# Kernel tuning notes

Measured on AMD Instinct MI355X. Metric: run time of the kernel, lower is better.

The kernel has to match this reference:

```python
import jax, jax.numpy as jnp
from jax import lax
import numpy as np

D_MODEL = 1024
EXPAND = 2
D_INNER = D_MODEL * EXPAND
D_STATE = 16
D_CONV = 4
DECAY = 0.95
LN_EPS = 1e-5


def setup_inputs() -> dict:
    key = jax.random.key(0)
    ks = jax.random.split(key, 9)
    b, s = 4, 2048
    scale = 1.0 / np.sqrt(D_MODEL)
    inner_scale = 1.0 / np.sqrt(D_INNER)
    return {
        "x": jax.random.normal(ks[0], (b, s, D_MODEL), dtype=jnp.float32),
        "W_in": jax.random.normal(ks[1], (2 * D_INNER, D_MODEL), dtype=jnp.float32) * scale,
        "conv_w": jax.random.normal(ks[2], (D_INNER, 1, D_CONV), dtype=jnp.float32) * 0.5,
        "conv_b": jax.random.normal(ks[3], (D_INNER,), dtype=jnp.float32) * 0.1,
        "W_x": jax.random.normal(ks[4], (2 * D_STATE, D_INNER), dtype=jnp.float32) * inner_scale,
        "B_log": jax.random.normal(ks[5], (D_INNER, D_STATE), dtype=jnp.float32) * 0.05,  # xavier-ish small
        "W_out": jax.random.normal(ks[6], (D_MODEL, D_INNER), dtype=jnp.float32) * inner_scale,
        "ln_g": jnp.ones((D_MODEL,), dtype=jnp.float32),
        "ln_b": jnp.zeros((D_MODEL,), dtype=jnp.float32),
    }


def _ssm_block(x, W_in, conv_w, conv_b, W_x, B_log, W_out, ln_g, ln_b):
    b, s, _ = x.shape
    d_inner = W_in.shape[0] // 2
    d_conv = conv_w.shape[-1]

    # input projection and gate split
    xz = jnp.einsum('bsd,ed->bse', x, W_in)            # [b, s, 2*d_inner]
    x_inner, z = jnp.split(xz, 2, axis=-1)             # each [b, s, d_inner]

    # causal depthwise conv (left pad d_conv-1, output length s)
    xc = jnp.transpose(x_inner, (0, 2, 1))             # [b, d_inner, s]
    conv = lax.conv_general_dilated(
        xc, conv_w, window_strides=(1,), padding=[(d_conv - 1, 0)],
        feature_group_count=d_inner)
    conv = conv + conv_b[None, :, None]
    x_conv = jax.nn.silu(jnp.transpose(conv, (0, 2, 1)))  # [b, s, d_inner]

    # selective parameters; s_B is produced but unused in the original math
    sp = jnp.einsum('bsd,nd->bsn', x_conv, W_x)        # [b, s, 2*d_state]
    _s_B, s_C = jnp.split(sp, 2, axis=-1)              # each [b, s, d_state]

    B = jnp.exp(B_log)                                  # [d_inner, d_state]

    # state_t = 0.95*state_{t-1} + B * x_t  factorizes as  state = B[d,n]*h[b,t,d]
    # with h_t = 0.95*h_{t-1} + x_conv_t ; scan over time with [b, d_inner] carry.
    def step(h, xt):
        h = DECAY * h + xt
        return h, h

    h0 = jnp.zeros((b, d_inner), dtype=x.dtype)
    _, h = lax.scan(step, h0, jnp.swapaxes(x_conv, 0, 1))  # [s, b, d_inner]
    h = jnp.swapaxes(h, 0, 1)                              # [b, s, d_inner]

    # output_t[b,d] = sum_n state[b,d,n]*s_C[b,t,n] = h[b,t,d] * (s_C @ B^T)[b,t,d]
    y = h * jnp.einsum('bsn,dn->bsd', s_C, B)
    y = y * jax.nn.silu(z)
    y = jnp.einsum('bsd,od->bso', y, W_out)            # [b, s, d_model]

    resid = x + y
    mu = jnp.mean(resid, axis=-1, keepdims=True)
    var = jnp.var(resid, axis=-1, keepdims=True)
    return (resid - mu) * lax.rsqrt(var + LN_EPS) * ln_g + ln_b


def reference(x, W_in, conv_w, conv_b, W_x, B_log, W_out, ln_g, ln_b):
    return _ssm_block(x, W_in, conv_w, conv_b, W_x, B_log, W_out, ln_g, ln_b)
```

## Files before the change

kernel.cpp:

```cpp
#include <hip/hip_runtime.h>
#include <hip/hip_bf16.h>
#include <stdint.h>

#define DM   1024
#define DI   2048
#define NST  16
#define BSZ  4
#define SLEN 2048
#define MROWS (BSZ*SLEN)
#define CHUNK 32
#define NCH  (SLEN/CHUNK)
#define DECAYF 0.95f
#define MB (size_t)1048576

typedef _Float16 f16;
typedef __attribute__((ext_vector_type(2))) _Float16 f16x2;
typedef __attribute__((ext_vector_type(4))) _Float16 f16x4;
typedef __attribute__((ext_vector_type(8))) _Float16 f16x8;
typedef __attribute__((ext_vector_type(4))) float f32x4;

__device__ __forceinline__ float silu_f(float v) { return v / (1.f + __expf(-v)); }

__device__ __forceinline__ void gload16(const f16* lds, const f16* g) {
  __builtin_amdgcn_global_load_lds((const __attribute__((address_space(1))) void*)g,
                                   (__attribute__((address_space(3))) void*)lds, 16, 0, 0);
}

#define NX4  (MROWS * DM / 4)
#define NWI4 (2 * DI * DM / 4)
#define NWO4 (DM * DI / 4)
#define NWX4 (NST * DI / 4)
#define NE4  (NST * DI / 4)
__global__ __launch_bounds__(256) void cvt_all(
    const float* __restrict__ x, const float* __restrict__ wi, const float* __restrict__ wo,
    const float* __restrict__ Wx, const float* __restrict__ B_log,
    f16* __restrict__ A1, f16* __restrict__ B1, f16* __restrict__ W2,
    f16* __restrict__ WxC, f16* __restrict__ expBT)
{
  int i = blockIdx.x * 256 + threadIdx.x;
  if (i < NX4 + NWI4 + NWO4 + NWX4) {
    const float* src; f16* dst; int j;
    if (i < NX4)                     { src = x;  dst = A1; j = i; }
    else if (i < NX4 + NWI4)         { src = wi; dst = B1; j = i - NX4; }
    else if (i < NX4 + NWI4 + NWO4)  { src = wo; dst = W2; j = i - NX4 - NWI4; }
    else                             { src = Wx + (size_t)NST * DI; dst = WxC; j = i - NX4 - NWI4 - NWO4; }
    float4 v = ((const float4*)src)[j];
    f16x4 o = {(f16)v.x, (f16)v.y, (f16)v.z, (f16)v.w};
    ((f16x4*)dst)[j] = o;
  } else {
    int j = i - NX4 - NWI4 - NWO4 - NWX4;
    int base = j * 4;
    int n = base >> 11, d = base & (DI - 1);
    f16x4 o = {(f16)__expf(B_log[(d + 0) * NST + n]), (f16)__expf(B_log[(d + 1) * NST + n]),
               (f16)__expf(B_log[(d + 2) * NST + n]), (f16)__expf(B_log[(d + 3) * NST + n])};
    ((f16x4*)expBT)[j] = o;
  }
}

#define G1K 1024

__device__ __forceinline__ void stage_t(const f16* __restrict__ mat, int matBase,
                                        int kt, f16* ldsDst, int tid) {
  #pragma unroll
  for (int q = 0; q < 2; ++q) {
    int c = q * 512 + tid;
    int row = c >> 2, p = c & 3;
    int su = p ^ ((row >> 1) & 3);
    gload16(ldsDst + c * 8, mat + (size_t)(matBase + row) * G1K + kt * 32 + su * 8);
  }
}

#define WAITV(n) asm volatile("s_waitcnt vmcnt(" #n ")" ::: "memory")

__global__ __launch_bounds__(512, 2) void gemm1_8ph(
    const f16* __restrict__ A, const f16* __restrict__ Bt,
    f16* __restrict__ Xi, f16* __restrict__ Zs)
{
  __shared__ __align__(16) f16 lds[65536];
  const int tid  = threadIdx.x;
  const int lane = tid & 63;
  const int w    = tid >> 6;
  const int wr   = w >> 2, wc = w & 3;
  const int lr   = lane & 15;
  const int lq   = lane >> 4;

  const int nwg = gridDim.x * gridDim.y;
  int wgid = blockIdx.y * gridDim.x + blockIdx.x;
  wgid = (wgid & 7) * (nwg >> 3) + (wgid >> 3);
  const int bx = wgid % gridDim.x;
  const int by = wgid / gridDim.x;
  const int mBase = by * 256;
  const int nBase = bx * 256;

  f32x4 acc[8][4];
  #pragma unroll
  for (int mf = 0; mf < 8; ++mf)
    #pragma unroll
    for (int nf = 0; nf < 4; ++nf)
      acc[mf][nf] = (f32x4){0.f, 0.f, 0.f, 0.f};

  auto rdA = [&](int S, int mf) -> f16x8 {
    int ra = wr * 128 + mf * 16 + lr;
    return *(const f16x8*)&lds[S + ra * 32 + (lq ^ ((ra >> 1) & 3)) * 8];
  };
  auto rdB = [&](int S, int nf) -> f16x8 {
    int rb = wc * 64 + nf * 16 + lr;
    return *(const f16x8*)&lds[S + 8192 + rb * 32 + (lq ^ ((rb >> 1) & 3)) * 8];
  };

  f16x8 bfr[4], afr[8];

#define PH(S, ISSUE, TAIL) do {                                                 \
    _Pragma("unroll")                                                           \
    for (int nf = 0; nf < 4; ++nf) bfr[nf] = rdB((S), nf);                      \
    _Pragma("unroll")                                                           \
    for (int mm = 0; mm < 8; ++mm) afr[mm] = rdA((S), mm);                      \
    ISSUE;                                                                      \
    __builtin_amdgcn_s_barrier();                                               \
    asm volatile("s_waitcnt lgkmcnt(0)" ::: "memory");                          \
    __builtin_amdgcn_sched_barrier(0);                                          \
    __builtin_amdgcn_s_setprio(1);                                              \
    _Pragma("unroll")                                                           \
    for (int mm = 0; mm < 8; ++mm)                                              \
      _Pragma("unroll")                                                         \
      for (int nf = 0; nf < 4; ++nf)                                            \
        acc[mm][nf] = __builtin_amdgcn_mfma_f32_16x16x32_f16(                   \
            afr[mm], bfr[nf], acc[mm][nf], 0, 0, 0);                            \
    __builtin_amdgcn_s_setprio(0);                                              \
    __builtin_amdgcn_sched_barrier(0);                                          \
    TAIL;                                                                       \
    __builtin_amdgcn_s_barrier();                                               \
  } while (0)

  stage_t(A,  mBase, 0, &lds[0],             tid);
  stage_t(Bt, nBase, 0, &lds[8192],          tid);
  stage_t(A,  mBase, 1, &lds[16384],         tid);
  stage_t(Bt, nBase, 1, &lds[16384 + 8192],  tid);
  stage_t(A,  mBase, 2, &lds[32768],         tid);
  stage_t(Bt, nBase, 2, &lds[32768 + 8192],  tid);
  WAITV(8);
  __builtin_amdgcn_s_barrier();

  #pragma unroll
  for (int T = 0; T < 32; ++T) {
    const int S = (T & 3) * 16384;
    const int F = ((T + 3) & 3) * 16384;
    PH(S,
       { if (T + 3 < 32) { stage_t(A, mBase, T + 3, &lds[F], tid);
                           stage_t(Bt, nBase, T + 3, &lds[F + 8192], tid); } },
       { if (T < 29) { WAITV(8); } else if (T == 29) { WAITV(4); } else if (T == 30) { WAITV(0); } });
  }
#undef PH

  __syncthreads();
  const int rq = lq * 4;
  #pragma unroll
  for (int mf = 0; mf < 8; ++mf)
    #pragma unroll
    for (int nf = 0; nf < 4; ++nf)
      #pragma unroll
      for (int r = 0; r < 4; ++r)
        lds[(wr * 128 + mf * 16 + rq + r) * 256 + wc * 64 + nf * 16 + lr] = (f16)acc[mf][nf][r];
  __syncthreads();
  #pragma unroll
  for (int it = 0; it < 16; ++it) {
    int cidx = it * 512 + tid;
    int row = cidx >> 5;
    int col8 = (cidx & 31) * 8;
    int grow = mBase + row;
    int gcol = nBase + col8;
    f16x8 v = *(const f16x8*)&lds[row * 256 + col8];
    if (gcol < DI) *(f16x8*)&Xi[(size_t)grow * DI + gcol] = v;
    else           *(f16x8*)&Zs[(size_t)grow * DI + (gcol - DI)] = v;
  }
}

template<int MODE>
__global__ __launch_bounds__(256) void gemm_bt(
    const f16* __restrict__ A, const f16* __restrict__ Bt,
    int K, f16* __restrict__ O0, f16* __restrict__ O1)
{
  __shared__ __align__(16) f16 sA[128 * 64];
  __shared__ __align__(16) f16 sB[128 * 64];
  const int tid  = threadIdx.x;
  const int lane = tid & 63;
  const int w    = tid >> 6;
  const int wr   = w >> 1, wc = w & 1;

  const int nwg  = gridDim.x * gridDim.y;
  int wgid = blockIdx.y * gridDim.x + blockIdx.x;
  wgid = (wgid & 7) * (nwg >> 3) + (wgid >> 3);
  const int bx = wgid % gridDim.x;
  const int by = wgid / gridDim.x;

  const int mBase = by * 128;
  const int nBase = bx * 128;
  const int lr = lane & 15;
  const int lu = lane >> 4;

  f32x4 acc[4][4];
  #pragma unroll
  for (int m = 0; m < 4; ++m)
    #pragma unroll
    for (int n = 0; n < 4; ++n)
      acc[m][n] = (f32x4){0.f, 0.f, 0.f, 0.f};

  int offA[4][2], offB[4][2];
  #pragma unroll
  for (int m = 0; m < 4; ++m) {
    int ra = wr * 64 + m * 16 + lr;
    int rb = wc * 64 + m * 16 + lr;
    #pragma unroll
    for (int kk = 0; kk < 2; ++kk) {
      offA[m][kk] = ra * 64 + ((kk * 4 + lu) ^ (ra & 7)) * 8;
      offB[m][kk] = rb * 64 + ((kk * 4 + lu) ^ (rb & 7)) * 8;
    }
  }

  for (int k0 = 0; k0 < K; k0 += 64) {
    #pragma unroll
    for (int j = 0; j < 4; ++j) {
      int c = j * 256 + tid;
      int row = c >> 3, p = c & 7;
      int su = p ^ (row & 7);
      gload16(&sA[c * 8], A  + (size_t)(mBase + row) * K + k0 + su * 8);
      gload16(&sB[c * 8], Bt + (size_t)(nBase + row) * K + k0 + su * 8);
    }
    __syncthreads();
    #pragma unroll
    for (int kk = 0; kk < 2; ++kk) {
      f16x8 af[4], bf[4];
      #pragma unroll
      for (int m = 0; m < 4; ++m) af[m] = *(const f16x8*)&sA[offA[m][kk]];
      #pragma unroll
      for (int n = 0; n < 4; ++n) bf[n] = *(const f16x8*)&sB[offB[n][kk]];
      #pragma unroll
      for (int m = 0; m < 4; ++m)
        #pragma unroll
        for (int n = 0; n < 4; ++n)
          acc[m][n] = __builtin_amdgcn_mfma_f32_16x16x32_f16(af[m], bf[n], acc[m][n], 0, 0, 0);
    }
    __syncthreads();
  }

  const int rq = (lane >> 4) * 4;
  f16* sOut = sA;
  const bool isZ = (MODE == 1) && (nBase >= DI);
  f16* dst = (MODE == 0) ? O0 : (isZ ? O1 : O0);
  const int ncols = (MODE == 0) ? DM : DI;
  const int cb = isZ ? (nBase - DI) : nBase;
  #pragma unroll
  for (int m = 0; m < 4; ++m) {
    #pragma unroll
    for (int n = 0; n < 4; ++n)
      #pragma unroll
      for (int r = 0; r < 4; ++r)
        sOut[(wr * 16 + rq + r) * 128 + wc * 64 + n * 16 + lr] = (f16)acc[m][n][r];
    __syncthreads();
    #pragma unroll
    for (int q = 0; q < 2; ++q) {
      int cidx = q * 256 + tid;
      int orow = cidx >> 4;
      int ocol = (cidx & 15) * 8;
      int grow = mBase + (orow >> 4) * 64 + m * 16 + (orow & 15);
      f16x8 v = *(const f16x8*)&sOut[orow * 128 + ocol];
      *(f16x8*)&dst[(size_t)grow * ncols + cb + ocol] = v;
    }
    __syncthreads();
  }
}

__global__ __launch_bounds__(256) void conv_scan(
    const f16* __restrict__ Xi, const float* __restrict__ convW, const float* __restrict__ convB,
    f16* __restrict__ Xc, f16* __restrict__ Hl, float* __restrict__ L)
{
  const int tid = threadIdx.x;
  const int d0 = (blockIdx.x * 256 + tid) * 4;
  const int ch = blockIdx.y;
  const int b  = blockIdx.z;
  const int t0 = ch * CHUNK;

  float w0[4], w1[4], w2[4], w3[4], cb[4];
  #pragma unroll
  for (int i = 0; i < 4; ++i) {
    float4 wv = ((const float4*)convW)[d0 + i];
    w0[i] = wv.x; w1[i] = wv.y; w2[i] = wv.z; w3[i] = wv.w;
    cb[i] = convB[d0 + i];
  }

  float xm3[4], xm2[4], xm1[4];
  auto loadrow = [&](int t, float* dst) {
    if (t < 0) {
      #pragma unroll
      for (int i = 0; i < 4; ++i) dst[i] = 0.f;
      return;
    }
    f16x4 v = *(const f16x4*)&Xi[((size_t)(b * SLEN + t)) * DI + d0];
    #pragma unroll
    for (int i = 0; i < 4; ++i) dst[i] = (float)v[i];
  };
  loadrow(t0 - 3, xm3); loadrow(t0 - 2, xm2); loadrow(t0 - 1, xm1);

  float h[4] = {0.f, 0.f, 0.f, 0.f};
  for (int t = 0; t < CHUNK; ++t) {
    const size_t ro = ((size_t)(b * SLEN + t0 + t)) * DI + d0;
    f16x4 xv = *(const f16x4*)&Xi[ro];
    f16x4 xco, hho;
    #pragma unroll
    for (int i = 0; i < 4; ++i) {
      float xt = (float)xv[i];
      float c = cb[i] + w0[i]*xm3[i] + w1[i]*xm2[i] + w2[i]*xm1[i] + w3[i]*xt;
      float xc = silu_f(c);
      h[i] = DECAYF * h[i] + xc;
      xco[i] = (f16)xc;
      hho[i] = (f16)h[i];
      xm3[i] = xm2[i]; xm2[i] = xm1[i]; xm1[i] = xt;
    }
    *(f16x4*)&Xc[ro] = xco;
    *(f16x4*)&Hl[ro] = hho;
  }
  const size_t lo = ((size_t)(b * NCH + ch)) * DI + d0;
  float4 l0 = {h[0], h[1], h[2], h[3]};
  *(float4*)&L[lo] = l0;
}

__global__ void carry_scan(const float* __restrict__ L, f16* __restrict__ Carry) {
  int i = blockIdx.x * blockDim.x + threadIdx.x;
  int b = i >> 11, d = i & (DI - 1);
  float dp = 1.f;
  #pragma unroll
  for (int k = 0; k < CHUNK; ++k) dp *= DECAYF;
  float c = 0.f;
  for (int ch0 = 0; ch0 < NCH; ch0 += 8) {
    float lv[8];
    #pragma unroll
    for (int k = 0; k < 8; ++k)
      lv[k] = L[((size_t)(b * NCH + ch0 + k)) * DI + d];
    #pragma unroll
    for (int k = 0; k < 8; ++k) {
      c = dp * c + lv[k];
      Carry[((size_t)(b * NCH + ch0 + k)) * DI + d] = (f16)c;
    }
  }
}

__global__ __launch_bounds__(256) void sc_gemm(const f16* __restrict__ Xc, const f16* __restrict__ WxC,
                                               float* __restrict__ sC) {
  const int m = blockIdx.x * 4 + (threadIdx.x >> 6);
  const int lane = threadIdx.x & 63;
  float acc[16];
  #pragma unroll
  for (int n = 0; n < 16; ++n) acc[n] = 0.f;
  #pragma unroll
  for (int it = 0; it < DI / 512; ++it) {
    int d = it * 512 + lane * 8;
    f16x8 xv = *(const f16x8*)&Xc[(size_t)m * DI + d];
    #pragma unroll
    for (int n = 0; n < 16; ++n) {
      f16x8 wv = *(const f16x8*)&WxC[(size_t)n * DI + d];
      float s = 0.f;
      #pragma unroll
      for (int i = 0; i < 8; ++i) s += (float)xv[i] * (float)wv[i];
      acc[n] += s;
    }
  }
  #pragma unroll
  for (int n = 0; n < 16; ++n) {
    #pragma unroll
    for (int off = 32; off > 0; off >>= 1) acc[n] += __shfl_xor(acc[n], off);
  }
  if (lane == 0) {
    #pragma unroll
    for (int n = 0; n < 16; ++n) sC[m * 16 + n] = acc[n];
  }
}

__global__ __launch_bounds__(256) void ew_y(
    const f16* __restrict__ Hl, const f16* __restrict__ Zs,
    const float* __restrict__ sC, const f16* __restrict__ expBT,
    const f16* __restrict__ Carry, f16* __restrict__ Y)
{
  const int r = threadIdx.x >> 6, lane = threadIdx.x & 63;
  const int m = blockIdx.y * 4 + r;
  const int d0 = blockIdx.x * 512 + lane * 8;
  const int b = m >> 11, t = m & (SLEN - 1);
  const int ch = t / CHUNK, tl = t & (CHUNK - 1);

  float coef = 0.f;
  if (ch > 0) {
    coef = 1.f;
    for (int j = 0; j <= tl; ++j) coef *= DECAYF;
  }

  const float4 sc0 = *(const float4*)&sC[m * 16 + 0];
  const float4 sc1 = *(const float4*)&sC[m * 16 + 4];
  const float4 sc2 = *(const float4*)&sC[m * 16 + 8];
  const float4 sc3 = *(const float4*)&sC[m * 16 + 12];
  const float scv[16] = {sc0.x, sc0.y, sc0.z, sc0.w, sc1.x, sc1.y, sc1.z, sc1.w,
                         sc2.x, sc2.y, sc2.z, sc2.w, sc3.x, sc3.y, sc3.z, sc3.w};

  const size_t ro = (size_t)m * DI + d0;
  f16x8 hvv = *(const f16x8*)&Hl[ro];
  f16x8 zvv = *(const f16x8*)&Zs[ro];
  float hv[8], zv[8], ca[8];
  #pragma unroll
  for (int i = 0; i < 8; ++i) {
    hv[i] = (float)hvv[i];
    zv[i] = silu_f((float)zvv[i]);
    ca[i] = 0.f;
  }
  if (ch > 0) {
    const size_t co = ((size_t)(b * NCH + ch - 1)) * DI + d0;
    f16x8 cv = *(const f16x8*)&Carry[co];
    #pragma unroll
    for (int i = 0; i < 8; ++i) ca[i] = (float)cv[i];
  }

  float cp[8] = {0.f, 0.f, 0.f, 0.f, 0.f, 0.f, 0.f, 0.f};
  #pragma unroll
  for (int n = 0; n < 16; ++n) {
    f16x8 ev = *(const f16x8*)&expBT[(size_t)n * DI + d0];
    #pragma unroll
    for (int i = 0; i < 8; ++i) cp[i] += scv[n] * (float)ev[i];
  }

  f16x8 o;
  #pragma unroll
  for (int i = 0; i < 8; ++i) {
    float y = (hv[i] + coef * ca[i]) * cp[i] * zv[i];
    o[i] = (f16)y;
  }
  *(f16x8*)&Y[ro] = o;
}

__global__ __launch_bounds__(256) void ln_res(const f16* __restrict__ G, const float* __restrict__ x,
                                              const float* __restrict__ lng, const float* __restrict__ lnb,
                                              float* __restrict__ out) {
  const int m = blockIdx.x;
  const int tid = threadIdx.x;
  f16x4 gv4 = ((const f16x4*)(G + (size_t)m * DM))[tid];
  float4 xv = ((const float4*)(x + (size_t)m * DM))[tid];
  float4 rv = {(float)gv4.x + xv.x, (float)gv4.y + xv.y, (float)gv4.z + xv.z, (float)gv4.w + xv.w};
  float s = rv.x + rv.y + rv.z + rv.w;
  float s2 = rv.x * rv.x + rv.y * rv.y + rv.z * rv.z + rv.w * rv.w;
  #pragma unroll
  for (int off = 32; off > 0; off >>= 1) {
    s += __shfl_xor(s, off);
    s2 += __shfl_xor(s2, off);
  }
  __shared__ float ps[8];
  const int w = tid >> 6;
  if ((tid & 63) == 0) { ps[w] = s; ps[w + 4] = s2; }
  __syncthreads();
  float S = ps[0] + ps[1] + ps[2] + ps[3];
  float S2 = ps[4] + ps[5] + ps[6] + ps[7];
  float mu = S * (1.f / DM);
  float var = S2 * (1.f / DM) - mu * mu;
  float rs = rsqrtf(var + 1e-5f);
  float4 gg = ((const float4*)lng)[tid];
  float4 bb = ((const float4*)lnb)[tid];
  float4 ov = {(rv.x - mu) * rs * gg.x + bb.x, (rv.y - mu) * rs * gg.y + bb.y,
               (rv.z - mu) * rs * gg.z + bb.z, (rv.w - mu) * rs * gg.w + bb.w};
  ((float4*)(out + (size_t)m * DM))[tid] = ov;
}

extern "C" void kernel_launch(void* const* d_in, const int* in_sizes, int n_in,
                              void* d_out, int out_size, void* d_ws, size_t ws_size,
                              hipStream_t stream) {
  const float* x      = (const float*)d_in[0];
  const float* W_in   = (const float*)d_in[1];
  const float* conv_w = (const float*)d_in[2];
  const float* conv_b = (const float*)d_in[3];
  const float* W_x    = (const float*)d_in[4];
  const float* B_log  = (const float*)d_in[5];
  const float* W_out  = (const float*)d_in[6];
  const float* ln_g   = (const float*)d_in[7];
  const float* ln_b   = (const float*)d_in[8];
  float* out = (float*)d_out;

  char* ws = (char*)d_ws;
  f16*   Xi  = (f16*)(ws + 0);
  f16*   Yp  = (f16*)(ws + 0);
  f16*   Zs  = (f16*)(ws + 32 * MB);
  f16*   Xc  = (f16*)(ws + 64 * MB);
  f16*   Hl  = (f16*)(ws + 96 * MB);
  f16*   A1  = (f16*)(ws + 128 * MB);
  f16*   B1  = (f16*)(ws + 144 * MB);
  f16*   W2  = (f16*)(ws + 152 * MB);
  f16*   G   = (f16*)(ws + 156 * MB);
  float* L     = (float*)(ws + 172 * MB);
  f16*   Carry = (f16*)(ws + 174 * MB);
  float* sC    = (float*)(ws + 175 * MB);
  f16*   expBT = (f16*)(ws + 176 * MB);
  f16*   WxC   = (f16*)(ws + 177 * MB);

  cvt_all<<<(NX4 + NWI4 + NWO4 + NWX4 + NE4) / 256, 256, 0, stream>>>(
      x, W_in, W_out, W_x, B_log, A1, B1, W2, WxC, expBT);

  gemm1_8ph<<<dim3(2 * DI / 256, MROWS / 256), 512, 0, stream>>>(A1, B1, Xi, Zs);

  conv_scan<<<dim3(DI / 1024, NCH, BSZ), 256, 0, stream>>>(Xi, conv_w, conv_b, Xc, Hl, L);
  carry_scan<<<(BSZ * DI) / 256, 256, 0, stream>>>(L, Carry);
  sc_gemm<<<MROWS / 4, 256, 0, stream>>>(Xc, WxC, sC);
  ew_y<<<dim3(DI / 512, MROWS / 4), 256, 0, stream>>>(Hl, Zs, sC, expBT, Carry, Yp);

  gemm_bt<0><<<dim3(DM / 128, MROWS / 128), 256, 0, stream>>>(Yp, W2, DI, G, nullptr);

  ln_res<<<MROWS, 256, 0, stream>>>(G, x, ln_g, ln_b, out);
}
```

Baseline: 252.4 us.

## Replace output GEMM with 4-stage pipelined 256x128 tile kernel

Replaces the simple synchronous 128x128 output-projection GEMM with a 512-thread kernel using 256x128 tiles and a 4-slot LDS ring buffer. Global loads are issued three K-steps ahead via direct-to-LDS loads, with explicit waitcnt, barriers and priority hints, so memory latency overlaps the MFMA work. This removes the per-iteration load-then-compute stall of the old kernel, but uses much more LDS per workgroup and halves the number of workgroups, which may lower occupancy.

Result: faster. 247.0 us (-2.1%).

```diff
diff --git a/kernel.cpp b/kernel.cpp
--- a/kernel.cpp
+++ b/kernel.cpp
@@ -175,98 +175,123 @@
   }
 }
 
-template<int MODE>
-__global__ __launch_bounds__(256) void gemm_bt(
-    const f16* __restrict__ A, const f16* __restrict__ Bt,
-    int K, f16* __restrict__ O0, f16* __restrict__ O1)
+#define G2K 2048
+#define SLOT2 12288
+
+__device__ __forceinline__ void stage2_A(const f16* __restrict__ mat, int mBase,
+                                         int kt, f16* ldsDst, int tid) {
+  #pragma unroll
+  for (int q = 0; q < 2; ++q) {
+    int c = q * 512 + tid;
+    int row = c >> 2, p = c & 3;
+    int su = p ^ ((row >> 1) & 3);
+    gload16(ldsDst + c * 8, mat + (size_t)(mBase + row) * G2K + kt * 32 + su * 8);
+  }
+}
+__device__ __forceinline__ void stage2_B(const f16* __restrict__ mat, int nBase,
+                                         int kt, f16* ldsDst, int tid) {
+  int c = tid;
+  int row = c >> 2, p = c & 3;
+  int su = p ^ ((row >> 1) & 3);
+  gload16(ldsDst + c * 8, mat + (size_t)(nBase + row) * G2K + kt * 32 + su * 8);
+}
+
+__global__ __launch_bounds__(512, 2) void gemm2_pipe(
+    const f16* __restrict__ A, const f16* __restrict__ Bt, f16* __restrict__ G)
 {
-  __shared__ __align__(16) f16 sA[128 * 64];
-  __shared__ __align__(16) f16 sB[128 * 64];
+  __shared__ __align__(16) f16 lds[49152];
   const int tid  = threadIdx.x;
   const int lane = tid & 63;
   const int w    = tid >> 6;
-  const int wr   = w >> 1, wc = w & 1;
-
-  const int nwg  = gridDim.x * gridDim.y;
+  const int wr   = w >> 2, wc = w & 3;
+  const int lr   = lane & 15;
+  const int lq   = lane >> 4;
+
+  const int nwg = gridDim.x * gridDim.y;
   int wgid = blockIdx.y * gridDim.x + blockIdx.x;
   wgid = (wgid & 7) * (nwg >> 3) + (wgid >> 3);
   const int bx = wgid % gridDim.x;
   const int by = wgid / gridDim.x;
-
-  const int mBase = by * 128;
+  const int mBase = by * 256;
   const int nBase = bx * 128;
-  const int lr = lane & 15;
-  const int lu = lane >> 4;
-
-  f32x4 acc[4][4];
-  #pragma unroll
-  for (int m = 0; m < 4; ++m)
-    #pragma unroll
-    for (int n = 0; n < 4; ++n)
-      acc[m][n] = (f32x4){0.f, 0.f, 0.f, 0.f};
-
-  int offA[4][2], offB[4][2];
-  #pragma unroll
-  for (int m = 0; m < 4; ++m) {
-    int ra = wr * 64 + m * 16 + lr;
-    int rb = wc * 64 + m * 16 + lr;
-    #pragma unroll
-    for (int kk = 0; kk < 2; ++kk) {
-      offA[m][kk] = ra * 64 + ((kk * 4 + lu) ^ (ra & 7)) * 8;
-      offB[m][kk] = rb * 64 + ((kk * 4 + lu) ^ (rb & 7)) * 8;
-    }
-  }
-
-  for (int k0 = 0; k0 < K; k0 += 64) {
-    #pragma unroll
-    for (int j = 0; j < 4; ++j) {
-      int c = j * 256 + tid;
-      int row = c >> 3, p = c & 7;
-      int su = p ^ (row & 7);
-      gload16(&sA[c * 8], A  + (size_t)(mBase + row) * K + k0 + su * 8);
-      gload16(&sB[c * 8], Bt + (size_t)(nBase + row) * K + k0 + su * 8);
-    }
-    __syncthreads();
-    #pragma unroll
-    for (int kk = 0; kk < 2; ++kk) {
-      f16x8 af[4], bf[4];
-      #pragma unroll
-      for (int m = 0; m < 4; ++m) af[m] = *(const f16x8*)&sA[offA[m][kk]];
-      #pragma unroll
-      for (int n = 0; n < 4; ++n) bf[n] = *(const f16x8*)&sB[offB[n][kk]];
-      #pragma unroll
-      for (int m = 0; m < 4; ++m)
-        #pragma unroll
-        for (int n = 0; n < 4; ++n)
-          acc[m][n] = __builtin_amdgcn_mfma_f32_16x16x32_f16(af[m], bf[n], acc[m][n], 0, 0, 0);
-    }
-    __syncthreads();
-  }
-
-  const int rq = (lane >> 4) * 4;
-  f16* sOut = sA;
-  const bool isZ = (MODE == 1) && (nBase >= DI);
-  f16* dst = (MODE == 0) ? O0 : (isZ ? O1 : O0);
-  const int ncols = (MODE == 0) ? DM : DI;
-  const int cb = isZ ? (nBase - DI) : nBase;
-  #pragma unroll
-  for (int m = 0; m < 4; ++m) {
-    #pragma unroll
-    for (int n = 0; n < 4; ++n)
+
+  f32x4 acc[8][2];
+  #pragma unroll
+  for (int mf = 0; mf < 8; ++mf)
+    #pragma unroll
+    for (int nf = 0; nf < 2; ++nf)
+      acc[mf][nf] = (f32x4){0.f, 0.f, 0.f, 0.f};
+
+  auto rdA = [&](int S, int mf) -> f16x8 {
+    int ra = wr * 128 + mf * 16 + lr;
+    return *(const f16x8*)&lds[S + ra * 32 + (lq ^ ((ra >> 1) & 3)) * 8];
+  };
+  auto rdB = [&](int S, int nf) -> f16x8 {
+    int rb = wc * 32 + nf * 16 + lr;
+    return *(const f16x8*)&lds[S + 8192 + rb * 32 + (lq ^ ((rb >> 1) & 3)) * 8];
+  };
+
+  f16x8 bfr[2], afr[8];
+
+#define PH2(S, ISSUE, TAIL) do {                                                \
+    _Pragma("unroll")                                                           \
+    for (int nf = 0; nf < 2; ++nf) bfr[nf] = rdB((S), nf);                      \
+    _Pragma("unroll")                                                           \
+    for (int mm = 0; mm < 8; ++mm) afr[mm] = rdA((S), mm);                      \
+    ISSUE;                                                                      \
+    __builtin_amdgcn_s_barrier();                                               \
+    asm volatile("s_waitcnt lgkmcnt(0)" ::: "memory");                          \
+    __builtin_amdgcn_sched_barrier(0);                                          \
+    __builtin_amdgcn_s_setprio(1);                                              \
+    _Pragma("unroll")                                                           \
+    for (int mm = 0; mm < 8; ++mm)                                              \
+      _Pragma("unroll")                                                         \
+      for (int nf = 0; nf < 2; ++nf)                                            \
+        acc[mm][nf] = __builtin_amdgcn_mfma_f32_16x16x32_f16(                   \
+            afr[mm], bfr[nf], acc[mm][nf], 0, 0, 0);                            \
+    __builtin_amdgcn_s_setprio(0);                                              \
+    __builtin_amdgcn_sched_barrier(0);                                          \
+    TAIL;                                                                       \
+    __builtin_amdgcn_s_barrier();                                               \
+  } while (0)
+
+  stage2_A(A,  mBase, 0, &lds[0],                 tid);
+  stage2_B(Bt, nBase, 0, &lds[8192],              tid);
+  stage2_A(A,  mBase, 1, &lds[SLOT2],             tid);
+  stage2_B(Bt, nBase, 1, &lds[SLOT2 + 8192],      tid);
+  stage2_A(A,  mBase, 2, &lds[2 * SLOT2],         tid);
+  stage2_B(Bt, nBase, 2, &lds[2 * SLOT2 + 8192],  tid);
+  WAITV(6);
+  __builtin_amdgcn_s_barrier();
+
+  #pragma unroll
+  for (int T = 0; T < 64; ++T) {
+    const int S = (T & 3) * SLOT2;
+    const int F = ((T + 3) & 3) * SLOT2;
+    PH2(S,
+        { if (T + 3 < 64) { stage2_A(A, mBase, T + 3, &lds[F], tid);
+                            stage2_B(Bt, nBase, T + 3, &lds[F + 8192], tid); } },
+        { if (T < 61) { WAITV(6); } else if (T == 61) { WAITV(3); } else if (T == 62) { WAITV(0); } });
+  }
+#undef PH2
+
+  __syncthreads();
+  const int rq = lq * 4;
+  #pragma unroll
+  for (int mf = 0; mf < 8; ++mf)
+    #pragma unroll
+    for (int nf = 0; nf < 2; ++nf)
       #pragma unroll
       for (int r = 0; r < 4; ++r)
-        sOut[(wr * 16 + rq + r) * 128 + wc * 64 + n * 16 + lr] = (f16)acc[m][n][r];
-    __syncthreads();
-    #pragma unroll
-    for (int q = 0; q < 2; ++q) {
-      int cidx = q * 256 + tid;
-      int orow = cidx >> 4;
-      int ocol = (cidx & 15) * 8;
-      int grow = mBase + (orow >> 4) * 64 + m * 16 + (orow & 15);
-      f16x8 v = *(const f16x8*)&sOut[orow * 128 + ocol];
-      *(f16x8*)&dst[(size_t)grow * ncols + cb + ocol] = v;
-    }
-    __syncthreads();
+        lds[(wr * 128 + mf * 16 + rq + r) * 128 + wc * 32 + nf * 16 + lr] = (f16)acc[mf][nf][r];
+  __syncthreads();
+  #pragma unroll
+  for (int it = 0; it < 8; ++it) {
+    int cidx = it * 512 + tid;
+    int row = cidx >> 4;
+    int col8 = (cidx & 15) * 8;
+    f16x8 v = *(const f16x8*)&lds[row * 128 + col8];
+    *(f16x8*)&G[(size_t)(mBase + row) * DM + nBase + col8] = v;
   }
 }
 
@@ -504,7 +529,7 @@
   sc_gemm<<<MROWS / 4, 256, 0, stream>>>(Xc, WxC, sC);
   ew_y<<<dim3(DI / 512, MROWS / 4), 256, 0, stream>>>(Hl, Zs, sC, expBT, Carry, Yp);
 
-  gemm_bt<0><<<dim3(DM / 128, MROWS / 128), 256, 0, stream>>>(Yp, W2, DI, G, nullptr);
+  gemm2_pipe<<<dim3(DM / 128, MROWS / 256), 512, 0, stream>>>(Yp, W2, G);
 
   ln_res<<<MROWS, 256, 0, stream>>>(G, x, ln_g, ln_b, out);
 }
```
